# Kernel tuning notes

Measured on AMD Instinct MI355X. Metric: run time of the kernel, lower is better.

Reference implementation:

```python
import jax, jax.numpy as jnp
import numpy as np
from fractions import Fraction
from math import factorial

MUL = 128
LS = [0, 1, 2]  # Rs_in1 = Rs_in2 = [(128,0),(128,1),(128,2)]
D_IN = MUL * sum(2 * l + 1 for l in LS)  # 1152
D_OUT = MUL * sum(2 * lo + 1 for l in LS for lo in range(2 * l + 1))  # 4480
N = 16384


def _su2_cg(j1, m1, j2, m2, j3, m3):
    # SU(2) Clebsch-Gordan coefficient (Racah formula), exact rational arithmetic.
    if m3 != m1 + m2:
        return 0.0
    f = lambda n: factorial(round(n))
    vmin = int(max(-j1 + j2 + m3, -j1 + m1, 0))
    vmax = int(min(j2 + j3 + m1, j3 - j1 + j2, j3 + m3))
    c = ((2.0 * j3 + 1.0) * Fraction(
        f(j3 + j1 - j2) * f(j3 - j1 + j2) * f(j1 + j2 - j3) * f(j3 + m3) * f(j3 - m3),
        f(j1 + j2 + j3 + 1) * f(j1 - m1) * f(j1 + m1) * f(j2 - m2) * f(j2 + m2))) ** 0.5
    s = 0
    for v in range(vmin, vmax + 1):
        s += (-1) ** (v + j2 + m2) * Fraction(
            f(j2 + j3 + m1 - v) * f(j1 - m1 + v),
            f(v) * f(j3 - j1 + j2 - v) * f(j3 + m3 - v) * f(v + j1 - j2 - m3))
    return float(c * s)


def _su2_tensor(j1, j2, j3):
    C = np.zeros((2 * j1 + 1, 2 * j2 + 1, 2 * j3 + 1))
    for m1 in range(-j1, j1 + 1):
        for m2 in range(-j2, j2 + 1):
            m3 = m1 + m2
            if abs(m3) <= j3:
                C[j1 + m1, j2 + m2, j3 + m3] = _su2_cg(j1, m1, j2, m2, j3, m3)
    return C


def _cb(l):
    # change of basis real -> complex spherical harmonics (e3nn convention, incl. (-i)^l phase)
    q = np.zeros((2 * l + 1, 2 * l + 1), dtype=np.complex128)
    for m in range(-l, 0):
        q[l + m, l + abs(m)] = 2 ** -0.5
        q[l + m, l - abs(m)] = -1j * 2 ** -0.5
    q[l, l] = 1.0
    for m in range(1, l + 1):
        q[l + m, l + abs(m)] = (-1) ** m * 2 ** -0.5
        q[l + m, l - abs(m)] = 1j * (-1) ** m * 2 ** -0.5
    return (-1j) ** l * q


def _wigner3j(l1, l2, l3):
    # real-basis Wigner 3j tensor, unit Frobenius norm (e3nn convention)
    C = _su2_tensor(l1, l2, l3).astype(np.complex128)
    C = np.einsum('ij,kl,mn,ikn->jlm', _cb(l1), _cb(l2), np.conj(_cb(l3).T), C)
    C = np.real(C)
    return C / np.linalg.norm(C)


# precomputed CG blocks with 'component' normalization: w3j(l_out, l, l) * sqrt(2*l_out+1)
CG = {(lo, l): jnp.asarray((_wigner3j(lo, l, l) * np.sqrt(2 * lo + 1)).astype(np.float32))
      for l in LS for lo in range(2 * l + 1)}


def _forward(features_1, features_2):
    # elementwise (channel-matched) tensor product, block-sparse CG contraction.
    # Equivalent to: outer(features_1, features_2) then sparse Wigner-3j mixing matmul,
    # but without materializing the [N, d1, d2] outer product.
    lead = features_1.shape[:-1]
    outs = []
    off = 0
    for l in LS:
        d = MUL * (2 * l + 1)
        b1 = features_1[..., off:off + d].reshape(*lead, MUL, 2 * l + 1)
        b2 = features_2[..., off:off + d].reshape(*lead, MUL, 2 * l + 1)
        for lo in range(2 * l + 1):  # selection_rule: l_out in |l-l|..2l, ascending
            o = jnp.einsum('kij,...ui,...uj->...uk', CG[(lo, l)], b1, b2)
            outs.append(o.reshape(*lead, MUL * (2 * lo + 1)))
        off += d
    return jnp.concatenate(outs, axis=-1)  # [..., D_OUT]


def setup_inputs() -> dict:
    key = jax.random.key(0)
    k1, k2 = jax.random.split(key)
    return {
        "features_1": jax.random.normal(k1, (N, D_IN), dtype=jnp.float32),
        "features_2": jax.random.normal(k2, (N, D_IN), dtype=jnp.float32),
    }


def reference(features_1, features_2):
    return _forward(features_1, features_2)
```

## Files before the change

### kernel.cpp

```cpp
#include <hip/hip_runtime.h>


#define NROW 16384
#define DIN  1152
#define DOUT 4480

__device__ float g_cgtab[707];

struct cd { double x, y; };
__device__ __forceinline__ cd cmul(cd a, cd b) {
    return cd{a.x * b.x - a.y * b.y, a.x * b.y + a.y * b.x};
}

__device__ __forceinline__ int imax(int a, int b) { return a > b ? a : b; }
__device__ __forceinline__ int imin(int a, int b) { return a < b ? a : b; }

__device__ double su2_cg_d(int j1, int m1, int j2, int m2, int j3, int m3,
                           const double* f) {
    if (m3 != m1 + m2) return 0.0;
    int vmin = imax(imax(-j1 + j2 + m3, -j1 + m1), 0);
    int vmax = imin(imin(j2 + j3 + m1, j3 - j1 + j2), j3 + m3);
    if (vmax < vmin) return 0.0;
    double c = sqrt((2.0 * j3 + 1.0) *
                    f[j3 + j1 - j2] * f[j3 - j1 + j2] * f[j1 + j2 - j3] *
                    f[j3 + m3] * f[j3 - m3] /
                    (f[j1 + j2 + j3 + 1] * f[j1 - m1] * f[j1 + m1] *
                     f[j2 - m2] * f[j2 + m2]));
    double s = 0.0;
    for (int v = vmin; v <= vmax; ++v) {
        double num = f[j2 + j3 + m1 - v] * f[j1 - m1 + v];
        double den = f[v] * f[j3 - j1 + j2 - v] * f[j3 + m3 - v] * f[v + j1 - j2 - m3];
        double term = num / den;
        s += ((v + j2 + m2) & 1) ? -term : term;
    }
    return c * s;
}

__device__ void fill_cb(int l, cd* q) {
    int d = 2 * l + 1;
    for (int i = 0; i < d * d; i++) q[i] = cd{0.0, 0.0};
    const double is2 = 0.70710678118654752440;
    for (int m = -l; m < 0; m++) {
        q[(l + m) * d + (l - m)] = cd{is2, 0.0};
        q[(l + m) * d + (l + m)] = cd{0.0, -is2};
    }
    q[l * d + l] = cd{1.0, 0.0};
    for (int m = 1; m <= l; m++) {
        double sg = (m & 1) ? -1.0 : 1.0;
        q[(l + m) * d + (l + m)] = cd{sg * is2, 0.0};
        q[(l + m) * d + (l - m)] = cd{0.0, sg * is2};
    }
    int ph = l & 3;
    for (int i = 0; i < d * d; i++) {
        cd z = q[i], r;
        if (ph == 0) r = z;
        else if (ph == 1) r = cd{z.y, -z.x};
        else if (ph == 2) r = cd{-z.x, -z.y};
        else r = cd{-z.y, z.x};
        q[i] = r;
    }
}

__global__ void cg_gen() {
    int b = blockIdx.x;
    int l = (b == 0) ? 0 : (b < 4 ? 1 : 2);
    int lo = (b == 0) ? 0 : (b < 4 ? b - 1 : b - 4);
    int base = (l == 0) ? 0 : (l == 1 ? 1 : 82);
    int d2 = 2 * l + 1, d1 = 2 * lo + 1;
    int off = base + d2 * d2 * lo * lo;
    int Nent = d1 * d2 * d2;

    __shared__ double fct[12];
    __shared__ double su2[225];
    __shared__ cd cb1[81];
    __shared__ cd cb2[25];
    __shared__ double val[225];

    if (threadIdx.x == 0) {
        fct[0] = 1.0;
        for (int i = 1; i < 12; i++) fct[i] = fct[i - 1] * i;
    }
    __syncthreads();

    for (int e = threadIdx.x; e < Nent; e += blockDim.x) {
        int i = e / (d2 * d2), r = e % (d2 * d2);
        int k = r / d2, n = r % d2;
        su2[e] = su2_cg_d(lo, i - lo, l, k - l, l, n - l, fct);
    }
    if (threadIdx.x == 0) { fill_cb(lo, cb1); fill_cb(l, cb2); }
    __syncthreads();

    for (int e = threadIdx.x; e < Nent; e += blockDim.x) {
        int jo = e / (d2 * d2), r = e % (d2 * d2);
        int kb = r / d2, mb = r % d2;
        double sx = 0.0;
        for (int i = 0; i < d1; i++) {
            cd c1 = cb1[i * d1 + jo];
            for (int k = 0; k < d2; k++) {
                cd c12 = cmul(c1, cb2[k * d2 + kb]);
                for (int n = 0; n < d2; n++) {
                    double cv = su2[(i * d2 + k) * d2 + n];
                    if (cv != 0.0) {
                        cd c3 = cb2[n * d2 + mb];
                        c3.y = -c3.y;
                        cd term = cmul(c12, c3);
                        sx += term.x * cv;
                    }
                }
            }
        }
        val[e] = sx;
    }
    __syncthreads();

    double ss = 0.0;
    for (int e = 0; e < Nent; e++) { double v = val[e]; ss += v * v; }
    double scale = sqrt((double)d1) / sqrt(ss);
    for (int e = threadIdx.x; e < Nent; e += blockDim.x)
        g_cgtab[off + e] = (float)(val[e] * scale);
}


template <int DO_, int DI>
__device__ __forceinline__ void contract1(const float* __restrict__ t,
                                          const float* a, const float* b,
                                          float* __restrict__ os, int ch) {
#pragma unroll
    for (int k = 0; k < DO_; k++) {
        float acc = 0.0f;
#pragma unroll
        for (int i = 0; i < DI; i++)
#pragma unroll
            for (int j = 0; j < DI; j++)
                acc = fmaf(t[(k * DI + i) * DI + j], a[i] * b[j], acc);
        os[ch * DO_ + k] = acc;
    }
}

__global__ __launch_bounds__(256, 4) void etp_main(
    const float* __restrict__ f1, const float* __restrict__ f2,
    float* __restrict__ out) {
    __shared__ float t[707];
    __shared__ alignas(16) float ostage[2][4096];

    for (int i = threadIdx.x; i < 707; i += 256) t[i] = g_cgtab[i];
    __syncthreads();

    const int rin = threadIdx.x >> 7;
    const int ch = threadIdx.x & 127;
    const size_t row = (size_t)blockIdx.x * 2 + rin;

    const float* __restrict__ p1 = f1 + row * DIN;
    const float* __restrict__ p2 = f2 + row * DIN;
    float* __restrict__ po = out + row * DOUT;
    float* __restrict__ os = ostage[rin];

    float a0 = p1[ch], b0 = p2[ch];
    float a1[3], b1[3];
#pragma unroll
    for (int k = 0; k < 3; k++) {
        a1[k] = p1[128 + ch * 3 + k];
        b1[k] = p2[128 + ch * 3 + k];
    }
    float a2[5], b2[5];
#pragma unroll
    for (int k = 0; k < 5; k++) {
        a2[k] = p1[512 + ch * 5 + k];
        b2[k] = p2[512 + ch * 5 + k];
    }

    po[ch] = t[0] * a0 * b0;
    {
        float s = 0.0f;
#pragma unroll
        for (int i = 0; i < 3; i++)
#pragma unroll
            for (int j = 0; j < 3; j++) s = fmaf(t[1 + i * 3 + j], a1[i] * b1[j], s);
        po[128 + ch] = s;
    }
    {
        float s = 0.0f;
#pragma unroll
        for (int i = 0; i < 5; i++)
#pragma unroll
            for (int j = 0; j < 5; j++) s = fmaf(t[82 + i * 5 + j], a2[i] * b2[j], s);
        po[1280 + ch] = s;
    }

    contract1<3, 3>(t + 10, a1, b1, os + 0, ch);
    contract1<5, 3>(t + 37, a1, b1, os + 384, ch);
    contract1<3, 5>(t + 107, a2, b2, os + 1024, ch);
    contract1<5, 5>(t + 182, a2, b2, os + 1408, ch);
    contract1<7, 5>(t + 307, a2, b2, os + 2048, ch);
    contract1<9, 5>(t + 482, a2, b2, os + 2944, ch);

    __syncthreads();

    const float4* __restrict__ src = reinterpret_cast<const float4*>(os);
    float4* __restrict__ dA = reinterpret_cast<float4*>(po + 256);
#pragma unroll
    for (int i = 0; i < 2; i++) dA[ch + 128 * i] = src[ch + 128 * i];
    float4* __restrict__ dB = reinterpret_cast<float4*>(po + 1408);
#pragma unroll
    for (int i = 0; i < 6; i++) dB[ch + 128 * i] = src[256 + ch + 128 * i];
}

extern "C" void kernel_launch(void* const* d_in, const int* in_sizes, int n_in,
                              void* d_out, int out_size, void* d_ws, size_t ws_size,
                              hipStream_t stream) {
    const float* f1 = (const float*)d_in[0];
    const float* f2 = (const float*)d_in[1];
    float* out = (float*)d_out;

    hipLaunchKernelGGL(cg_gen, dim3(9), dim3(256), 0, stream);
    hipLaunchKernelGGL(etp_main, dim3(NROW / 2), dim3(256), 0, stream,
                       f1, f2, out);
}
```

Baseline: 436.3 us.

## Split each row's channel work across two thread halves with precomputed outer products

Each block now handles one row instead of two. The first 128 threads compute the l=0, l=1 and l=2→9 outputs, and the second 128 threads compute the remaining l=2 outputs, which balances the FMA work per thread. The outer products a_i*b_j are formed once per channel and reused across output components. The CG table is read directly from global memory instead of being staged in LDS, and launch bounds rise to 6 blocks. This risks more redundant global loads of the l=2 inputs, some divergence between the two thread groups, and register pressure from the 25-element product array.

```diff
diff --git a/kernel.cpp b/kernel.cpp
--- a/kernel.cpp
+++ b/kernel.cpp
@@ -121,88 +121,101 @@
 }
 
 
-template <int DO_, int DI>
-__device__ __forceinline__ void contract1(const float* __restrict__ t,
-                                          const float* a, const float* b,
-                                          float* __restrict__ os, int ch) {
+template <int DO_, int NE>
+__device__ __forceinline__ void contractP(const float* __restrict__ t,
+                                          const float* q,
+                                          float* __restrict__ os) {
 #pragma unroll
     for (int k = 0; k < DO_; k++) {
         float acc = 0.0f;
 #pragma unroll
-        for (int i = 0; i < DI; i++)
-#pragma unroll
-            for (int j = 0; j < DI; j++)
-                acc = fmaf(t[(k * DI + i) * DI + j], a[i] * b[j], acc);
-        os[ch * DO_ + k] = acc;
-    }
-}
-
-__global__ __launch_bounds__(256, 4) void etp_main(
+        for (int e = 0; e < NE; e++) acc = fmaf(t[k * NE + e], q[e], acc);
+        os[k] = acc;
+    }
+}
+
+__global__ __launch_bounds__(256, 6) void etp_main(
     const float* __restrict__ f1, const float* __restrict__ f2,
     float* __restrict__ out) {
-    __shared__ float t[707];
-    __shared__ alignas(16) float ostage[2][4096];
-
-    for (int i = threadIdx.x; i < 707; i += 256) t[i] = g_cgtab[i];
-    __syncthreads();
-
-    const int rin = threadIdx.x >> 7;
-    const int ch = threadIdx.x & 127;
-    const size_t row = (size_t)blockIdx.x * 2 + rin;
+    __shared__ alignas(16) float os[4096];
+    const float* __restrict__ t = g_cgtab;
+
+    const int tid = threadIdx.x;
+    const int ch = tid & 127;
+    const size_t row = blockIdx.x;
 
     const float* __restrict__ p1 = f1 + row * DIN;
     const float* __restrict__ p2 = f2 + row * DIN;
     float* __restrict__ po = out + row * DOUT;
-    float* __restrict__ os = ostage[rin];
-
-    float a0 = p1[ch], b0 = p2[ch];
-    float a1[3], b1[3];
-#pragma unroll
-    for (int k = 0; k < 3; k++) {
-        a1[k] = p1[128 + ch * 3 + k];
-        b1[k] = p2[128 + ch * 3 + k];
-    }
-    float a2[5], b2[5];
-#pragma unroll
-    for (int k = 0; k < 5; k++) {
-        a2[k] = p1[512 + ch * 5 + k];
-        b2[k] = p2[512 + ch * 5 + k];
-    }
-
-    po[ch] = t[0] * a0 * b0;
-    {
-        float s = 0.0f;
+
+    if (tid < 128) {
+        float a0 = p1[ch], b0 = p2[ch];
+        float a1[3], b1[3];
+#pragma unroll
+        for (int k = 0; k < 3; k++) {
+            a1[k] = p1[128 + ch * 3 + k];
+            b1[k] = p2[128 + ch * 3 + k];
+        }
+        float a2[5], b2[5];
+#pragma unroll
+        for (int k = 0; k < 5; k++) {
+            a2[k] = p1[512 + ch * 5 + k];
+            b2[k] = p2[512 + ch * 5 + k];
+        }
+
+        po[ch] = t[0] * a0 * b0;
+
+        float q1[9];
 #pragma unroll
         for (int i = 0; i < 3; i++)
 #pragma unroll
-            for (int j = 0; j < 3; j++) s = fmaf(t[1 + i * 3 + j], a1[i] * b1[j], s);
-        po[128 + ch] = s;
-    }
-    {
-        float s = 0.0f;
+            for (int j = 0; j < 3; j++) q1[i * 3 + j] = a1[i] * b1[j];
+        {
+            float s = 0.0f;
+#pragma unroll
+            for (int e = 0; e < 9; e++) s = fmaf(t[1 + e], q1[e], s);
+            po[128 + ch] = s;
+        }
+        contractP<3, 9>(t + 10, q1, os + 0 + ch * 3);
+        contractP<5, 9>(t + 37, q1, os + 384 + ch * 5);
+
+        float q2[25];
 #pragma unroll
         for (int i = 0; i < 5; i++)
 #pragma unroll
-            for (int j = 0; j < 5; j++) s = fmaf(t[82 + i * 5 + j], a2[i] * b2[j], s);
-        po[1280 + ch] = s;
-    }
-
-    contract1<3, 3>(t + 10, a1, b1, os + 0, ch);
-    contract1<5, 3>(t + 37, a1, b1, os + 384, ch);
-    contract1<3, 5>(t + 107, a2, b2, os + 1024, ch);
-    contract1<5, 5>(t + 182, a2, b2, os + 1408, ch);
-    contract1<7, 5>(t + 307, a2, b2, os + 2048, ch);
-    contract1<9, 5>(t + 482, a2, b2, os + 2944, ch);
+            for (int j = 0; j < 5; j++) q2[i * 5 + j] = a2[i] * b2[j];
+        contractP<9, 25>(t + 482, q2, os + 2944 + ch * 9);
+    } else {
+        float a2[5], b2[5];
+#pragma unroll
+        for (int k = 0; k < 5; k++) {
+            a2[k] = p1[512 + ch * 5 + k];
+            b2[k] = p2[512 + ch * 5 + k];
+        }
+        float q2[25];
+#pragma unroll
+        for (int i = 0; i < 5; i++)
+#pragma unroll
+            for (int j = 0; j < 5; j++) q2[i * 5 + j] = a2[i] * b2[j];
+        {
+            float s = 0.0f;
+#pragma unroll
+            for (int e = 0; e < 25; e++) s = fmaf(t[82 + e], q2[e], s);
+            po[1280 + ch] = s;
+        }
+        contractP<3, 25>(t + 107, q2, os + 1024 + ch * 3);
+        contractP<5, 25>(t + 182, q2, os + 1408 + ch * 5);
+        contractP<7, 25>(t + 307, q2, os + 2048 + ch * 7);
+    }
 
     __syncthreads();
 
     const float4* __restrict__ src = reinterpret_cast<const float4*>(os);
     float4* __restrict__ dA = reinterpret_cast<float4*>(po + 256);
-#pragma unroll
-    for (int i = 0; i < 2; i++) dA[ch + 128 * i] = src[ch + 128 * i];
     float4* __restrict__ dB = reinterpret_cast<float4*>(po + 1408);
-#pragma unroll
-    for (int i = 0; i < 6; i++) dB[ch + 128 * i] = src[256 + ch + 128 * i];
+    dA[tid] = src[tid];
+#pragma unroll
+    for (int i = 1; i < 4; i++) dB[tid + 256 * (i - 1)] = src[tid + 256 * i];
 }
 
 extern "C" void kernel_launch(void* const* d_in, const int* in_sizes, int n_in,
@@ -213,6 +226,6 @@
     float* out = (float*)d_out;
 
     hipLaunchKernelGGL(cg_gen, dim3(9), dim3(256), 0, stream);
-    hipLaunchKernelGGL(etp_main, dim3(NROW / 2), dim3(256), 0, stream,
+    hipLaunchKernelGGL(etp_main, dim3(NROW), dim3(256), 0, stream,
                        f1, f2, out);
 }
```

After: 428.2 us. Within noise of the previous version (-1.9%).
